# Kernel optimization log

Hardware: AMD Instinct MI355X
Metric: run time of the kernel (lower is better)

The kernel has to match this reference:

```python
import jax, jax.numpy as jnp
import numpy as np
from jax import lax

DT = 0.042
LIF_TAU_M = 20.0
THETA_LIF = 0.05
THETA_RF = 0.05
SPIKE_GAIN = 35.0
TAU_REF = 0.25
REF_DECAY = float(np.exp(-DT / TAU_REF))

B, L, N_INP, N_HID = 32, 512, 1, 1024
RHO = 0.99
INPUT_SCALING = 1.0
GAMMA_RANGE = (2.7, 4.7)
EPS_RANGE = (4.7, 6.7)


def setup_inputs() -> dict:
    key = jax.random.key(0)
    k_x, k_h, k_i, k_b, k_g, k_e = jax.random.split(key, 6)
    x = jax.random.normal(k_x, (B, L, N_INP), dtype=jnp.float32)
    # recurrent weights: 2*(2*U-1) then spectral-radius scaling to rho
    h2h = 2.0 * (2.0 * np.asarray(jax.random.uniform(k_h, (N_HID, N_HID))) - 1.0)
    sr = np.max(np.abs(np.linalg.eigvals(h2h)))
    h2h = jnp.asarray(h2h * (RHO / sr), dtype=jnp.float32)
    x2h = jax.random.uniform(k_i, (N_INP, N_HID), dtype=jnp.float32) * INPUT_SCALING
    bias = (jax.random.uniform(k_b, (N_HID,), dtype=jnp.float32) * 2.0 - 1.0) * 0.2 + 0.05
    gamma = jax.random.uniform(k_g, (N_HID,), dtype=jnp.float32) * (GAMMA_RANGE[1] - GAMMA_RANGE[0]) + GAMMA_RANGE[0]
    epsilon = jax.random.uniform(k_e, (N_HID,), dtype=jnp.float32) * (EPS_RANGE[1] - EPS_RANGE[0]) + EPS_RANGE[0]
    return {"x": x, "x2h": x2h, "h2h": h2h, "bias": bias, "gamma": gamma, "epsilon": epsilon}


def reference(x, x2h, h2h, bias, gamma, epsilon):
    dtype = x.dtype
    b, seq_len, _ = x.shape
    n_hid = h2h.shape[0]
    z0 = jnp.zeros((b, n_hid), dtype=dtype)
    # carry: (hy, hz, s, ref_period, lif_v)
    def step(carry, xt):
        hy, hz, s, ref_period, lif_v = carry
        # input current: external drive + recurrent spike drive + bias
        cur = xt @ x2h + s @ h2h + bias  # (B, n_hid)
        lif_v = lif_v + DT * (-lif_v / LIF_TAU_M + cur)
        lif_s = (lif_v > THETA_LIF).astype(dtype)
        lif_v = lif_v - lif_s * THETA_LIF  # soft (subtractive) reset
        # HRF oscillator driven by LIF spikes (alpha = beta = 0 -> no post-spike reset)
        hz = hz + DT * (SPIKE_GAIN * lif_s - gamma * hy - epsilon * hz)
        hy = hy + DT * hz
        s_new = (hy - THETA_RF - ref_period > 0).astype(dtype)
        ref_period = ref_period * REF_DECAY + s_new
        return (hy, hz, s_new, ref_period, lif_v), s_new

    carry0 = (z0, z0, z0, z0, z0)
    _, spikes = lax.scan(step, carry0, jnp.swapaxes(x, 0, 1))  # spikes: (L, B, n_hid)
    return spikes.mean(axis=0)  # mean firing rates (B, n_hid)
```

## Files before the change

### kernel.cpp

```cpp
#include <hip/hip_runtime.h>
#include <math.h>

#define NHID    1024
#define NSTEP   512
#define NB      32
#define NSPLIT  8
#define COLS    128
#define THREADS 512
#define NWAVES  8
#define MWORDS  32

__global__ __launch_bounds__(THREADS, 2)
void coesn_kernel(const float* __restrict__ x,
                  const float* __restrict__ x2h,
                  const float* __restrict__ h2h,
                  const float* __restrict__ bias,
                  const float* __restrict__ gamma_,
                  const float* __restrict__ eps_,
                  float* __restrict__ out,
                  unsigned long long* __restrict__ masks,
                  const float* __restrict__ zrow,
                  float ref_decay)
{
#pragma clang fp contract(off)
    const int tid  = threadIdx.x;
    const int blk  = blockIdx.x;
    const int b    = blk & 31;
    const int j    = blk >> 5;
    const int w    = tid >> 6;
    const int lane = tid & 63;

    __shared__ float xs[NSTEP];
    __shared__ unsigned short idxs[NHID + 128];
    __shared__ float part[NWAVES][COLS];
    __shared__ int   tot_sh[2];

    for (int i = tid; i < NSTEP; i += THREADS) xs[i] = x[b * NSTEP + i];

    float w_in = 0.f, bi = 0.f, ga = 0.f, ep = 0.f;
    if (tid < COLS) {
        int col = j * COLS + tid;
        w_in = x2h[col]; bi = bias[col]; ga = gamma_[col]; ep = eps_[col];
    }

    float hy = 0.f, hz = 0.f, ref = 0.f, lv = 0.f;
    int scount = 0;

    const int cb = j * COLS;
    const float* hrow_lane = h2h + cb + 2 * lane;
    const float* zlane     = zrow + 2 * lane;

    __syncthreads();

    for (int t = 0; t < NSTEP; ++t) {
        int total = 0, tot_pad = 0;
        int inc = 0, myc = 0;
        unsigned int myw = 0;

        if (t > 0) {
            const int par = (t - 1) & 1;
            if (tid < MWORDS) {
                const unsigned long long tag = (unsigned long long)t;
                unsigned long long v;
                int spin = 0;
                for (;;) {
                    v = __hip_atomic_load(&masks[(par * NB + b) * MWORDS + tid],
                                          __ATOMIC_RELAXED,
                                          __HIP_MEMORY_SCOPE_AGENT);
                    if ((v >> 32) == tag) break;
                    __builtin_amdgcn_s_sleep(1);
                    if (((++spin) & 4095) == 4095) {
                        (void)__hip_atomic_load(
                            &masks[(par * NB + b) * MWORDS + tid],
                            __ATOMIC_ACQUIRE, __HIP_MEMORY_SCOPE_AGENT);
                    }
                }
                myw = (unsigned int)v;
                myc = __popc(myw);
            }
            inc = myc;
            if (w == 0) {
                #pragma unroll
                for (int d = 1; d < 32; d <<= 1) {
                    int y = __shfl_up(inc, d, 64);
                    if (lane >= d) inc += y;
                }
                if (lane == 31) {
                    tot_sh[0] = inc;
                    tot_sh[1] = (inc + 127) & ~127;
                }
            }
            __syncthreads();
            total = tot_sh[0]; tot_pad = tot_sh[1];
            if (tid < MWORDS) {
                int off = inc - myc;
                int base = tid << 5;
                unsigned int wv = myw;
                while (wv) {
                    int bit = __builtin_ctz(wv);
                    idxs[off++] = (unsigned short)(base + bit);
                    wv &= wv - 1u;
                }
            }
            for (int i = total + tid; i < tot_pad; i += THREADS)
                idxs[i] = 1024;
            __syncthreads();
        }

        float ax = 0.f, ay = 0.f;
        for (int k = w; k < tot_pad; k += 128) {
            int r[16];
            #pragma unroll
            for (int u = 0; u < 16; ++u)
                r[u] = __builtin_amdgcn_readfirstlane((int)idxs[k + 8 * u]);
            const float* p[16];
            #pragma unroll
            for (int u = 0; u < 16; ++u)
                p[u] = (r[u] < 1024) ? (hrow_lane + ((size_t)r[u] << 10))
                                     : zlane;
            float2 v[16];
            #pragma unroll
            for (int u = 0; u < 16; ++u) v[u] = *(const float2*)p[u];
            #pragma unroll
            for (int u = 0; u < 16; ++u) { ax += v[u].x; ay += v[u].y; }
        }
        ((float2*)part[w])[lane] = make_float2(ax, ay);
        __syncthreads();

        if (tid < COLS) {
            float rsum = 0.f;
            #pragma unroll
            for (int ww = 0; ww < NWAVES; ++ww) rsum += part[ww][tid];

            float xv  = xs[t];
            float pp  = xv * w_in;
            float q   = pp + rsum;
            float cur = q + bi;

            float aa = (-lv) / 20.0f;
            float bb = aa + cur;
            lv = lv + 0.042f * bb;
            float ls = (lv > 0.05f) ? 1.0f : 0.0f;
            lv = lv - ls * 0.05f;

            float t1 = 35.0f * ls;
            float t2 = ga * hy;
            float t3 = ep * hz;
            float t4 = (t1 - t2) - t3;
            hz = hz + 0.042f * t4;
            hy = hy + 0.042f * hz;

            float sv = (hy - 0.05f) - ref;
            int sp = (sv > 0.0f) ? 1 : 0;
            ref = ref * ref_decay + (sp ? 1.0f : 0.0f);
            scount += sp;

            if (t < NSTEP - 1) {
                unsigned long long bal = __ballot(sp);
                if ((tid & 31) == 0) {
                    unsigned int half = (tid & 32) ? (unsigned int)(bal >> 32)
                                                   : (unsigned int)bal;
                    unsigned long long payload =
                        (((unsigned long long)(t + 1)) << 32) | half;
                    const int par = t & 1;
                    __hip_atomic_store(
                        &masks[(par * NB + b) * MWORDS + (j * 4 + (tid >> 5))],
                        payload, __ATOMIC_RELAXED, __HIP_MEMORY_SCOPE_AGENT);
                }
            }
        }
    }

    if (tid < COLS)
        out[b * NHID + cb + tid] = (float)scount * (1.0f / 512.0f);
}

extern "C" void kernel_launch(void* const* d_in, const int* in_sizes, int n_in,
                              void* d_out, int out_size, void* d_ws, size_t ws_size,
                              hipStream_t stream) {
    const float* x     = (const float*)d_in[0];
    const float* x2h   = (const float*)d_in[1];
    const float* h2h   = (const float*)d_in[2];
    const float* bias  = (const float*)d_in[3];
    const float* gamma = (const float*)d_in[4];
    const float* eps   = (const float*)d_in[5];
    float* out = (float*)d_out;

    unsigned long long* masks = (unsigned long long*)d_ws;
    const float* zrow = (const float*)((char*)d_ws + 16384);

    hipMemsetAsync(d_ws, 0, 24576, stream);

    float ref_decay = (float)exp(-(0.042 / 0.25));

    coesn_kernel<<<NB * NSPLIT, THREADS, 0, stream>>>(
        x, x2h, h2h, bias, gamma, eps, out, masks, zrow, ref_decay);
}
```

Before: 2.339 ms.

## Per-wave spike index compaction with buffer loads, removing per-step barriers

Each wave now reads only its own 4 mask words (a 128-row slice) and builds its own compacted index list with shuffles and popcounts. This removes the block-wide prefix scan and the two __syncthreads per timestep. Gathers go through raw buffer_load_dwordx2 with a buffer descriptor sized to h2h, so padded 1024 indices fall out of range and return zero; this replaces the zero-row workspace. The partial-sum buffer is double-buffered to avoid a second barrier, and launch bounds drop to one block per CU. The risks are load imbalance across waves, since each wave now handles a fixed row slice, and reliance on buffer out-of-bounds semantics.

Result: no change. 2.336 ms (-0.2%).

```diff
diff --git a/kernel.cpp b/kernel.cpp
--- a/kernel.cpp
+++ b/kernel.cpp
@@ -10,7 +10,10 @@
 #define NWAVES  8
 #define MWORDS  32
 
-__global__ __launch_bounds__(THREADS, 2)
+typedef float f2 __attribute__((ext_vector_type(2)));
+typedef int  v4i __attribute__((vector_size(16)));
+
+__global__ __launch_bounds__(THREADS, 1)
 void coesn_kernel(const float* __restrict__ x,
                   const float* __restrict__ x2h,
                   const float* __restrict__ h2h,
@@ -19,7 +22,6 @@
                   const float* __restrict__ eps_,
                   float* __restrict__ out,
                   unsigned long long* __restrict__ masks,
-                  const float* __restrict__ zrow,
                   float ref_decay)
 {
 #pragma clang fp contract(off)
@@ -31,9 +33,8 @@
     const int lane = tid & 63;
 
     __shared__ float xs[NSTEP];
-    __shared__ unsigned short idxs[NHID + 128];
-    __shared__ float part[NWAVES][COLS];
-    __shared__ int   tot_sh[2];
+    __shared__ unsigned short idxs[NWAVES][160];
+    __shared__ float part[2][NWAVES][COLS];
 
     for (int i = tid; i < NSTEP; i += THREADS) xs[i] = x[b * NSTEP + i];
 
@@ -43,94 +44,97 @@
         w_in = x2h[col]; bi = bias[col]; ga = gamma_[col]; ep = eps_[col];
     }
 
+    union { const float* p; unsigned int u[2]; } cv; cv.p = h2h;
+    v4i srd = { (int)cv.u[0], (int)(cv.u[1] & 0xffffu),
+                (int)(NHID * NHID * 4), 0x00020000 };
+
+    const unsigned cbase = (unsigned)(j * COLS * 4 + lane * 8);
+
     float hy = 0.f, hz = 0.f, ref = 0.f, lv = 0.f;
     int scount = 0;
-
-    const int cb = j * COLS;
-    const float* hrow_lane = h2h + cb + 2 * lane;
-    const float* zlane     = zrow + 2 * lane;
 
     __syncthreads();
 
     for (int t = 0; t < NSTEP; ++t) {
-        int total = 0, tot_pad = 0;
-        int inc = 0, myc = 0;
-        unsigned int myw = 0;
+        const int par = t & 1;
+        int npad = 0;
 
         if (t > 0) {
-            const int par = (t - 1) & 1;
-            if (tid < MWORDS) {
-                const unsigned long long tag = (unsigned long long)t;
-                unsigned long long v;
+            const int rpar = (t - 1) & 1;
+            unsigned long long v = 0;
+            if (lane < 4) {
+                const unsigned long long* ap =
+                    &masks[((size_t)rpar * NB + b) * MWORDS + (w << 2) + lane];
                 int spin = 0;
                 for (;;) {
-                    v = __hip_atomic_load(&masks[(par * NB + b) * MWORDS + tid],
-                                          __ATOMIC_RELAXED,
+                    v = __hip_atomic_load(ap, __ATOMIC_RELAXED,
                                           __HIP_MEMORY_SCOPE_AGENT);
-                    if ((v >> 32) == tag) break;
+                    if ((int)(v >> 32) == t) break;
                     __builtin_amdgcn_s_sleep(1);
-                    if (((++spin) & 4095) == 4095) {
-                        (void)__hip_atomic_load(
-                            &masks[(par * NB + b) * MWORDS + tid],
-                            __ATOMIC_ACQUIRE, __HIP_MEMORY_SCOPE_AGENT);
-                    }
-                }
-                myw = (unsigned int)v;
-                myc = __popc(myw);
-            }
-            inc = myc;
-            if (w == 0) {
-                #pragma unroll
-                for (int d = 1; d < 32; d <<= 1) {
-                    int y = __shfl_up(inc, d, 64);
-                    if (lane >= d) inc += y;
-                }
-                if (lane == 31) {
-                    tot_sh[0] = inc;
-                    tot_sh[1] = (inc + 127) & ~127;
+                    if (((++spin) & 4095) == 4095)
+                        (void)__hip_atomic_load(ap, __ATOMIC_ACQUIRE,
+                                                __HIP_MEMORY_SCOPE_AGENT);
                 }
             }
-            __syncthreads();
-            total = tot_sh[0]; tot_pad = tot_sh[1];
-            if (tid < MWORDS) {
-                int off = inc - myc;
-                int base = tid << 5;
-                unsigned int wv = myw;
-                while (wv) {
-                    int bit = __builtin_ctz(wv);
-                    idxs[off++] = (unsigned short)(base + bit);
-                    wv &= wv - 1u;
-                }
+            unsigned int hv = (unsigned int)v;
+            unsigned int m0 = (unsigned)__shfl((int)hv, 0, 64);
+            unsigned int m1 = (unsigned)__shfl((int)hv, 1, 64);
+            unsigned int m2 = (unsigned)__shfl((int)hv, 2, 64);
+            unsigned int m3 = (unsigned)__shfl((int)hv, 3, 64);
+            unsigned long long lo = (unsigned long long)m0 |
+                                    ((unsigned long long)m1 << 32);
+            unsigned long long hi = (unsigned long long)m2 |
+                                    ((unsigned long long)m3 << 32);
+            int cw = __popcll(lo) + __popcll(hi);
+            npad = (cw + 15) & ~15;
+
+            int p0 = lane << 1;
+            int c0, bit0, bit1;
+            if (lane < 32) {
+                c0   = __popcll(lo & ((1ull << p0) - 1ull));
+                bit0 = (int)((lo >> p0) & 1ull);
+                bit1 = (int)((lo >> (p0 + 1)) & 1ull);
+            } else {
+                int q0 = p0 - 64;
+                c0   = __popcll(lo) + __popcll(hi & ((1ull << q0) - 1ull));
+                bit0 = (int)((hi >> q0) & 1ull);
+                bit1 = (int)((hi >> (q0 + 1)) & 1ull);
             }
-            for (int i = total + tid; i < tot_pad; i += THREADS)
-                idxs[i] = 1024;
-            __syncthreads();
+            int rowbase = w << 7;
+            if (bit0) idxs[w][c0]        = (unsigned short)(rowbase + p0);
+            if (bit1) idxs[w][c0 + bit0] = (unsigned short)(rowbase + p0 + 1);
+            if (lane < npad - cw)
+                idxs[w][cw + lane] = (unsigned short)1024;
         }
 
-        float ax = 0.f, ay = 0.f;
-        for (int k = w; k < tot_pad; k += 128) {
-            int r[16];
+        f2 ax = {0.f, 0.f};
+        for (int k = 0; k < npad; k += 16) {
+            const uint4* qp = (const uint4*)&idxs[w][k];
+            uint4 qa = qp[0], qb = qp[1];
+            unsigned rr[16];
+            rr[0]=qa.x&0xffffu; rr[1]=qa.x>>16; rr[2]=qa.y&0xffffu; rr[3]=qa.y>>16;
+            rr[4]=qa.z&0xffffu; rr[5]=qa.z>>16; rr[6]=qa.w&0xffffu; rr[7]=qa.w>>16;
+            rr[8]=qb.x&0xffffu; rr[9]=qb.x>>16; rr[10]=qb.y&0xffffu; rr[11]=qb.y>>16;
+            rr[12]=qb.z&0xffffu; rr[13]=qb.z>>16; rr[14]=qb.w&0xffffu; rr[15]=qb.w>>16;
+            f2 vv[16];
             #pragma unroll
-            for (int u = 0; u < 16; ++u)
-                r[u] = __builtin_amdgcn_readfirstlane((int)idxs[k + 8 * u]);
-            const float* p[16];
+            for (int u = 0; u < 16; ++u) {
+                unsigned voff = (rr[u] << 12) + cbase;
+                asm volatile("buffer_load_dwordx2 %0, %1, %2, 0 offen"
+                             : "=v"(vv[u]) : "v"(voff), "s"(srd));
+            }
+            asm volatile("s_waitcnt vmcnt(0)" ::: "memory");
+            __builtin_amdgcn_sched_barrier(0);
             #pragma unroll
-            for (int u = 0; u < 16; ++u)
-                p[u] = (r[u] < 1024) ? (hrow_lane + ((size_t)r[u] << 10))
-                                     : zlane;
-            float2 v[16];
-            #pragma unroll
-            for (int u = 0; u < 16; ++u) v[u] = *(const float2*)p[u];
-            #pragma unroll
-            for (int u = 0; u < 16; ++u) { ax += v[u].x; ay += v[u].y; }
+            for (int u = 0; u < 16; ++u) { ax.x += vv[u].x; ax.y += vv[u].y; }
         }
-        ((float2*)part[w])[lane] = make_float2(ax, ay);
+        *(f2*)&part[par][w][lane << 1] = ax;
         __syncthreads();
 
         if (tid < COLS) {
             float rsum = 0.f;
             #pragma unroll
-            for (int ww = 0; ww < NWAVES; ++ww) rsum += part[ww][tid];
+            for (int ww = 0; ww < NWAVES; ++ww) rsum += part[par][ww][tid];
 
             float xv  = xs[t];
             float pp  = xv * w_in;
@@ -162,9 +166,8 @@
                                                    : (unsigned int)bal;
                     unsigned long long payload =
                         (((unsigned long long)(t + 1)) << 32) | half;
-                    const int par = t & 1;
                     __hip_atomic_store(
-                        &masks[(par * NB + b) * MWORDS + (j * 4 + (tid >> 5))],
+                        &masks[((size_t)par * NB + b) * MWORDS + (j << 2) + (tid >> 5)],
                         payload, __ATOMIC_RELAXED, __HIP_MEMORY_SCOPE_AGENT);
                 }
             }
@@ -172,7 +175,7 @@
     }
 
     if (tid < COLS)
-        out[b * NHID + cb + tid] = (float)scount * (1.0f / 512.0f);
+        out[b * NHID + j * COLS + tid] = (float)scount * (1.0f / 512.0f);
 }
 
 extern "C" void kernel_launch(void* const* d_in, const int* in_sizes, int n_in,
@@ -187,12 +190,10 @@
     float* out = (float*)d_out;
 
     unsigned long long* masks = (unsigned long long*)d_ws;
-    const float* zrow = (const float*)((char*)d_ws + 16384);
-
-    hipMemsetAsync(d_ws, 0, 24576, stream);
+    hipMemsetAsync(d_ws, 0, 16384, stream);
 
     float ref_decay = (float)exp(-(0.042 / 0.25));
 
     coesn_kernel<<<NB * NSPLIT, THREADS, 0, stream>>>(
-        x, x2h, h2h, bias, gamma, eps, out, masks, zrow, ref_decay);
+        x, x2h, h2h, bias, gamma, eps, out, masks, ref_decay);
 }
```
